# Kernel tuning notes

Measured on AMD Instinct MI355X. Metric: run time of the kernel, lower is better.

## Reference

```python
import jax, jax.numpy as jnp
import numpy as np

C = 1024
KSIZE = 7
PAD = 3
STRIDE = 1


def _dwconv(x, w):
    # x: [B, C, L], w: [C, 1, K] depthwise (feature_group_count=C)
    return jax.lax.conv_general_dilated(
        x, w,
        window_strides=(STRIDE,),
        padding=[(PAD, PAD)],
        feature_group_count=C,
        dimension_numbers=('NCH', 'OIH', 'NCH'),
    )


def setup_inputs() -> dict:
    key = jax.random.key(0)
    kx, kq, kk, kv = jax.random.split(key, 4)
    B, L = 8, 4096
    x = jax.random.normal(kx, (B, C, L), dtype=jnp.float32)
    # depthwise conv weights, fan_in = 1*K per group -> kaiming-ish scale
    scale = 1.0 / np.sqrt(KSIZE)
    q_w = jax.random.normal(kq, (C, 1, KSIZE), dtype=jnp.float32) * scale
    k_w = jax.random.normal(kk, (C, 1, KSIZE), dtype=jnp.float32) * scale
    v_w = jax.random.normal(kv, (C, 1, KSIZE), dtype=jnp.float32) * scale
    return {"x": x, "q_w": q_w, "k_w": k_w, "v_w": v_w}


def reference(x, q_w, k_w, v_w):
    sqrt_dk = np.sqrt(C).astype(np.float32)
    q = _dwconv(x, q_w)  # [B, C, L']
    k = _dwconv(x, k_w)
    v = _dwconv(x, v_w)
    score = jnp.einsum('bcl,bdl->bcd', q, k) / sqrt_dk  # [B, C, C]
    attn = jax.nn.softmax(score, axis=-1)
    out = jnp.einsum('bcd,bdl->bcl', attn, v)  # [B, C, L']
    return out
```

## Files before the change

### kernel.cpp

```cpp
#include <hip/hip_runtime.h>
#include <hip/hip_bf16.h>

typedef unsigned short u16;
typedef __attribute__((ext_vector_type(8))) __bf16 bf16x8;
typedef __attribute__((ext_vector_type(4))) float f32x4;

#define CC 1024
#define LL 4096
#define NB 8

#define VMCNT(n) asm volatile("s_waitcnt vmcnt(" #n ")" ::: "memory")
#define BAR()    asm volatile("s_barrier" ::: "memory")

__device__ __forceinline__ u16 f2bf(float f) {
  union { float f; unsigned u; } v; v.f = f;
  unsigned u = v.u;
  return (u16)((u + 0x7fffu + ((u >> 16) & 1u)) >> 16);
}

__device__ __forceinline__ void gload_lds16(const void* g, void* l) {
  __builtin_amdgcn_global_load_lds(
      (const __attribute__((address_space(1))) void*)g,
      (__attribute__((address_space(3))) void*)l, 16, 0, 0);
}

__global__ __launch_bounds__(256) void dwconv_qkv(
    const float* __restrict__ x, const float* __restrict__ qw,
    const float* __restrict__ kw, const float* __restrict__ vw,
    u16* __restrict__ qo, u16* __restrict__ ko, u16* __restrict__ vto)
{
  __shared__ u16 vs[64][66];
  const int t  = threadIdx.x;
  const int l0 = blockIdx.x << 6;
  const int c0 = blockIdx.y << 6;
  const int b  = blockIdx.z;
  const int cc  = t >> 2;
  const int li0 = (t & 3) << 4;
  const int c   = c0 + cc;
  const float* xr = x + ((size_t)(b * CC + c)) * LL;
  const int p0 = l0 + li0;

  float xv[24];
  if (l0 != 0 && l0 != LL - 64) {
    const float4* base = (const float4*)(xr + p0 - 4);
#pragma unroll
    for (int j = 0; j < 6; ++j) {
      float4 f = base[j];
      xv[4 * j + 0] = f.x; xv[4 * j + 1] = f.y;
      xv[4 * j + 2] = f.z; xv[4 * j + 3] = f.w;
    }
  } else {
#pragma unroll
    for (int i = 0; i < 24; ++i) {
      int gl = p0 - 4 + i;
      xv[i] = ((unsigned)gl < (unsigned)LL) ? xr[gl] : 0.f;
    }
  }

  float wq[7], wk[7], wv[7];
#pragma unroll
  for (int j = 0; j < 7; ++j) {
    wq[j] = qw[c * 7 + j]; wk[j] = kw[c * 7 + j]; wv[j] = vw[c * 7 + j];
  }

  alignas(16) u16 qv[16], kv[16];
#pragma unroll
  for (int li = 0; li < 16; ++li) {
    float aq = 0.f, ak = 0.f, av = 0.f;
#pragma unroll
    for (int j = 0; j < 7; ++j) {
      float xf = xv[li + 1 + j];
      aq = fmaf(xf, wq[j], aq);
      ak = fmaf(xf, wk[j], ak);
      av = fmaf(xf, wv[j], av);
    }
    qv[li] = f2bf(aq);
    kv[li] = f2bf(ak);
    vs[li0 + li][cc] = f2bf(av);
  }
  size_t qoff = ((size_t)(b * CC + c)) * LL + p0;
  *(uint4*)(qo + qoff)     = ((const uint4*)qv)[0];
  *(uint4*)(qo + qoff + 8) = ((const uint4*)qv)[1];
  *(uint4*)(ko + qoff)     = ((const uint4*)kv)[0];
  *(uint4*)(ko + qoff + 8) = ((const uint4*)kv)[1];

  __syncthreads();
  const int ll = t >> 2;
  const int cg = (t & 3) << 4;
  alignas(16) u16 vr[16];
#pragma unroll
  for (int j = 0; j < 16; ++j) vr[j] = vs[ll][cg + j];
  size_t voff = ((size_t)(b * LL + l0 + ll)) * CC + c0 + cg;
  *(uint4*)(vto + voff)     = ((const uint4*)vr)[0];
  *(uint4*)(vto + voff + 8) = ((const uint4*)vr)[1];
}

__global__ __launch_bounds__(512, 2) void gemm256p(
    const u16* __restrict__ A, int lda, size_t sA,
    const u16* __restrict__ B, int ldb, size_t sB,
    float* __restrict__ C0, float* __restrict__ C1, int ldc, size_t sC,
    int K, int ksplit, int mapmode)
{
  __shared__ alignas(16) u16 lds[65536];
  const int t    = threadIdx.x;
  const int lane = t & 63, wave = t >> 6;
  const int wrow = wave >> 2, wcol = wave & 3;
  int bx, by, z;
  if (mapmode == 0) {
    int wg = blockIdx.x; z = wg & 15; int r = wg >> 4; bx = r & 3; by = r >> 2;
  } else {
    int wg = blockIdx.x; z = wg & 7; by = (wg >> 3) & 3; bx = wg >> 5;
  }
  const int bm = by << 8, bn = bx << 8;
  const int batch = (ksplit == 2) ? (z >> 1) : z;
  const int split = (ksplit == 2) ? (z & 1) : 0;
  const int Ks    = (ksplit == 2) ? (K >> 1) : K;
  const u16* Ab = A + (size_t)batch * sA + (size_t)split * Ks;
  const u16* Bb = B + (size_t)batch * sB + (size_t)split * Ks;

  const int srow = lane >> 3;
  const int scol = ((lane & 7) ^ srow) << 3;
  const u16* pA[2][2]; const u16* pB[2][2];
  int dstOff[2];
#pragma unroll
  for (int i = 0; i < 2; ++i) {
    int c = wave * 2 + i;
    dstOff[i] = c * 1024 + lane * 16;
    pA[0][i] = Ab + (size_t)(bm + c * 8 + srow) * lda + scol;
    pA[1][i] = pA[0][i] + (size_t)128 * lda;
    pB[0][i] = Bb + (size_t)(bn + c * 8 + srow) * ldb + scol;
    pB[1][i] = pB[0][i] + (size_t)128 * ldb;
  }

#define STGH(P, h, base, koff)                                            \
  do {                                                                    \
    gload_lds16(P[h][0] + (koff), (char*)lds + (base) + dstOff[0]);       \
    gload_lds16(P[h][1] + (koff), (char*)lds + (base) + dstOff[1]);       \
  } while (0)

  const int r15 = lane & 15, kq = lane >> 4, swz = r15 & 7;
  int rowA[8], rowB[4], colK[2];
#pragma unroll
  for (int m = 0; m < 8; ++m) rowA[m] = (wrow * 128 + m * 16 + r15) * 128;
#pragma unroll
  for (int n = 0; n < 4; ++n) rowB[n] = 32768 + (wcol * 64 + n * 16 + r15) * 128;
#pragma unroll
  for (int s = 0; s < 2; ++s) colK[s] = (((s * 4 + kq) ^ swz)) << 4;

  f32x4 acc[8][4];
#pragma unroll
  for (int i = 0; i < 8; ++i)
#pragma unroll
    for (int j = 0; j < 4; ++j) acc[i][j] = f32x4{0.f, 0.f, 0.f, 0.f};

  const int NT = Ks >> 6;

  STGH(pA, 0, 0, 0);            STGH(pA, 1, 16384, 0);
  STGH(pB, 0, 32768, 0);        STGH(pB, 1, 49152, 0);
  STGH(pA, 0, 65536 + 0, 64);   STGH(pA, 1, 65536 + 16384, 64);
  STGH(pB, 0, 65536 + 32768, 64);
  VMCNT(6);
  BAR();

  const char* L = (const char*)lds;
  for (int tt = 0; tt < NT; ++tt) {
    const int d = tt & 1;
    const int dbase = d << 16, sbase = (d ^ 1) << 16;
    const int kN1 = (tt + 1) << 6, kN2 = (tt + 2) << 6;
    bf16x8 a0[4], aK1a[4], b0[4];
#pragma unroll
    for (int m = 0; m < 4; ++m) {
      a0[m]   = *(const bf16x8*)(L + dbase + rowA[m] + colK[0]);
      aK1a[m] = *(const bf16x8*)(L + dbase + rowA[m] + colK[1]);
    }
#pragma unroll
    for (int n = 0; n < 4; ++n) b0[n] = *(const bf16x8*)(L + dbase + rowB[n] + colK[0]);
    if (tt + 1 < NT) STGH(pB, 1, sbase + 49152, kN1);
    __builtin_amdgcn_s_setprio(1);
#pragma unroll
    for (int m = 0; m < 4; ++m)
#pragma unroll
      for (int n = 0; n < 4; ++n)
        acc[m][n] = __builtin_amdgcn_mfma_f32_16x16x32_bf16(a0[m], b0[n], acc[m][n], 0, 0, 0);
    __builtin_amdgcn_s_setprio(0);
    bf16x8 a4[4], aK1b[4];
#pragma unroll
    for (int m = 0; m < 4; ++m) {
      a4[m]   = *(const bf16x8*)(L + dbase + rowA[m + 4] + colK[0]);
      aK1b[m] = *(const bf16x8*)(L + dbase + rowA[m + 4] + colK[1]);
    }
    __builtin_amdgcn_s_setprio(1);
#pragma unroll
    for (int m = 0; m < 4; ++m)
#pragma unroll
      for (int n = 0; n < 4; ++n)
        acc[m + 4][n] = __builtin_amdgcn_mfma_f32_16x16x32_bf16(a4[m], b0[n], acc[m + 4][n], 0, 0, 0);
    __builtin_amdgcn_s_setprio(0);
    BAR();
    bf16x8 b1[4];
#pragma unroll
    for (int n = 0; n < 4; ++n) b1[n] = *(const bf16x8*)(L + dbase + rowB[n] + colK[1]);
    if (tt + 2 < NT) STGH(pA, 0, dbase + 0, kN2);
    __builtin_amdgcn_s_setprio(1);
#pragma unroll
    for (int m = 0; m < 4; ++m)
#pragma unroll
      for (int n = 0; n < 4; ++n)
        acc[m][n] = __builtin_amdgcn_mfma_f32_16x16x32_bf16(aK1a[m], b1[n], acc[m][n], 0, 0, 0);
    __builtin_amdgcn_s_setprio(0);
    BAR();
    if (tt + 2 < NT) { STGH(pA, 1, dbase + 16384, kN2); STGH(pB, 0, dbase + 32768, kN2); }
    __builtin_amdgcn_s_setprio(1);
#pragma unroll
    for (int m = 0; m < 4; ++m)
#pragma unroll
      for (int n = 0; n < 4; ++n)
        acc[m + 4][n] = __builtin_amdgcn_mfma_f32_16x16x32_bf16(aK1b[m], b1[n], acc[m + 4][n], 0, 0, 0);
    __builtin_amdgcn_s_setprio(0);
    if (tt < NT - 2) { VMCNT(6); } else { VMCNT(0); }
    BAR();
  }
#undef STGH

  float* Cb = (split ? C1 : C0) + (size_t)batch * sC;
  const int row0 = bm + wrow * 128 + kq * 4;
  const int col0 = bn + wcol * 64 + r15;
#pragma unroll
  for (int m = 0; m < 8; ++m)
#pragma unroll
    for (int n = 0; n < 4; ++n) {
      const int r   = row0 + m * 16;
      const int col = col0 + n * 16;
#pragma unroll
      for (int rr = 0; rr < 4; ++rr)
        Cb[(size_t)(r + rr) * ldc + col] = acc[m][n][rr];
    }
}

__global__ __launch_bounds__(256) void softmax_rows(
    float* __restrict__ score, const float* __restrict__ part)
{
  __shared__ float rmax[4], rsum[4];
  const int t = threadIdx.x;
  const int lane = t & 63, wv = t >> 6;
  float* sp = score + ((size_t)blockIdx.x << 10);
  const float* pp = part + ((size_t)blockIdx.x << 10);
  float4 v = ((const float4*)sp)[t];
  float4 w = ((const float4*)pp)[t];
  const float scale = 0.03125f;
  float a0 = (v.x + w.x) * scale, a1 = (v.y + w.y) * scale;
  float a2 = (v.z + w.z) * scale, a3 = (v.w + w.w) * scale;
  float m = fmaxf(fmaxf(a0, a1), fmaxf(a2, a3));
#pragma unroll
  for (int o = 1; o < 64; o <<= 1) m = fmaxf(m, __shfl_xor(m, o, 64));
  if (lane == 0) rmax[wv] = m;
  __syncthreads();
  m = fmaxf(fmaxf(rmax[0], rmax[1]), fmaxf(rmax[2], rmax[3]));
  float e0 = __expf(a0 - m), e1 = __expf(a1 - m);
  float e2 = __expf(a2 - m), e3 = __expf(a3 - m);
  float s = e0 + e1 + e2 + e3;
#pragma unroll
  for (int o = 1; o < 64; o <<= 1) s += __shfl_xor(s, o, 64);
  if (lane == 0) rsum[wv] = s;
  __syncthreads();
  s = rsum[0] + rsum[1] + rsum[2] + rsum[3];
  const float inv = 1.0f / s;
  union { u16 u[4]; uint2 p; } ob;
  ob.u[0] = f2bf(e0 * inv); ob.u[1] = f2bf(e1 * inv);
  ob.u[2] = f2bf(e2 * inv); ob.u[3] = f2bf(e3 * inv);
  *(uint2*)((u16*)sp + (t << 2)) = ob.p;
}

extern "C" void kernel_launch(void* const* d_in, const int* in_sizes, int n_in,
                              void* d_out, int out_size, void* d_ws, size_t ws_size,
                              hipStream_t stream) {
  const float* x  = (const float*)d_in[0];
  const float* qw = (const float*)d_in[1];
  const float* kw = (const float*)d_in[2];
  const float* vw = (const float*)d_in[3];
  float* out = (float*)d_out;
  char* ws = (char*)d_ws;

  u16*  q      = (u16*)ws;
  u16*  k      = (u16*)(ws + 67108864);
  u16*  vt     = (u16*)(ws + 134217728);
  float* score = (float*)(ws + 201326592);
  float* part  = out;

  dim3 cg(LL / 64, CC / 64, NB);
  dwconv_qkv<<<cg, 256, 0, stream>>>(x, qw, kw, vw, q, k, vt);

  gemm256p<<<dim3(256), 512, 0, stream>>>(q, LL, (size_t)CC * LL,
                                          k, LL, (size_t)CC * LL,
                                          score, part, CC, (size_t)CC * CC,
                                          LL, 2, 0);

  softmax_rows<<<NB * CC, 256, 0, stream>>>(score, part);

  gemm256p<<<dim3(512), 512, 0, stream>>>((const u16*)score, 2048, (size_t)CC * 2048,
                                          vt, CC, (size_t)LL * CC,
                                          out, nullptr, LL, (size_t)CC * LL,
                                          CC, 1, 1);
}
```

Measured before the change: 251.5 us.

## Widen dwconv tiles, swizzle V transpose, use hardware bf16 convert and nontemporal stores

The depthwise conv kernel now covers 128 sequence positions per block instead of 64, with 32 outputs per thread. This cuts halo reloads and the number of blocks. The shared-memory transpose for V uses an XOR swizzle on 16-column groups to reduce bank conflicts, and each thread writes 64-byte rows of V^T. The manual bf16 rounding is replaced with the compiler's native conversion. Q, K, V^T and the GEMM outputs are written with nontemporal stores to reduce cache pollution, at the cost of more registers per thread and possibly worse reuse when later kernels read the data.

Result: slower. 466.1 us (+85.4%).

```diff
diff --git a/kernel.cpp b/kernel.cpp
--- a/kernel.cpp
+++ b/kernel.cpp
@@ -4,6 +4,7 @@
 typedef unsigned short u16;
 typedef __attribute__((ext_vector_type(8))) __bf16 bf16x8;
 typedef __attribute__((ext_vector_type(4))) float f32x4;
+typedef __attribute__((ext_vector_type(4))) unsigned int u32x4;
 
 #define CC 1024
 #define LL 4096
@@ -16,6 +17,11 @@
   union { float f; unsigned u; } v; v.f = f;
   unsigned u = v.u;
   return (u16)((u + 0x7fffu + ((u >> 16) & 1u)) >> 16);
+}
+
+__device__ __forceinline__ u16 bfc(float f) {
+  __bf16 h = (__bf16)f;
+  return __builtin_bit_cast(u16, h);
 }
 
 __device__ __forceinline__ void gload_lds16(const void* g, void* l) {
@@ -29,29 +35,29 @@
     const float* __restrict__ kw, const float* __restrict__ vw,
     u16* __restrict__ qo, u16* __restrict__ ko, u16* __restrict__ vto)
 {
-  __shared__ u16 vs[64][66];
+  __shared__ u16 vs[128][68];
   const int t  = threadIdx.x;
-  const int l0 = blockIdx.x << 6;
+  const int l0 = blockIdx.x << 7;
   const int c0 = blockIdx.y << 6;
   const int b  = blockIdx.z;
-  const int cc  = t >> 2;
-  const int li0 = (t & 3) << 4;
-  const int c   = c0 + cc;
+  const int cc = t >> 2;
+  const int g  = t & 3;
+  const int c  = c0 + cc;
   const float* xr = x + ((size_t)(b * CC + c)) * LL;
-  const int p0 = l0 + li0;
-
-  float xv[24];
-  if (l0 != 0 && l0 != LL - 64) {
+  const int p0 = l0 + (g << 5);
+
+  float xv[40];
+  if (l0 != 0 && l0 != LL - 128) {
     const float4* base = (const float4*)(xr + p0 - 4);
 #pragma unroll
-    for (int j = 0; j < 6; ++j) {
+    for (int j = 0; j < 10; ++j) {
       float4 f = base[j];
       xv[4 * j + 0] = f.x; xv[4 * j + 1] = f.y;
       xv[4 * j + 2] = f.z; xv[4 * j + 3] = f.w;
     }
   } else {
 #pragma unroll
-    for (int i = 0; i < 24; ++i) {
+    for (int i = 0; i < 40; ++i) {
       int gl = p0 - 4 + i;
       xv[i] = ((unsigned)gl < (unsigned)LL) ? xr[gl] : 0.f;
     }
@@ -63,9 +69,10 @@
     wq[j] = qw[c * 7 + j]; wk[j] = kw[c * 7 + j]; wv[j] = vw[c * 7 + j];
   }
 
-  alignas(16) u16 qv[16], kv[16];
-#pragma unroll
-  for (int li = 0; li < 16; ++li) {
+  const int wgrp = cc >> 4;
+  alignas(16) u16 qv[32], kv[32];
+#pragma unroll
+  for (int li = 0; li < 32; ++li) {
     float aq = 0.f, ak = 0.f, av = 0.f;
 #pragma unroll
     for (int j = 0; j < 7; ++j) {
@@ -74,25 +81,33 @@
       ak = fmaf(xf, wk[j], ak);
       av = fmaf(xf, wv[j], av);
     }
-    qv[li] = f2bf(aq);
-    kv[li] = f2bf(ak);
-    vs[li0 + li][cc] = f2bf(av);
+    qv[li] = bfc(aq);
+    kv[li] = bfc(ak);
+    vs[(g << 5) + li][(cc & 15) + ((wgrp ^ g) << 4)] = bfc(av);
   }
   size_t qoff = ((size_t)(b * CC + c)) * LL + p0;
-  *(uint4*)(qo + qoff)     = ((const uint4*)qv)[0];
-  *(uint4*)(qo + qoff + 8) = ((const uint4*)qv)[1];
-  *(uint4*)(ko + qoff)     = ((const uint4*)kv)[0];
-  *(uint4*)(ko + qoff + 8) = ((const uint4*)kv)[1];
+#pragma unroll
+  for (int h = 0; h < 4; ++h) {
+    __builtin_nontemporal_store(((const u32x4*)qv)[h], (u32x4*)(qo + qoff) + h);
+    __builtin_nontemporal_store(((const u32x4*)kv)[h], (u32x4*)(ko + qoff) + h);
+  }
 
   __syncthreads();
-  const int ll = t >> 2;
-  const int cg = (t & 3) << 4;
-  alignas(16) u16 vr[16];
-#pragma unroll
-  for (int j = 0; j < 16; ++j) vr[j] = vs[ll][cg + j];
-  size_t voff = ((size_t)(b * LL + l0 + ll)) * CC + c0 + cg;
-  *(uint4*)(vto + voff)     = ((const uint4*)vr)[0];
-  *(uint4*)(vto + voff + 8) = ((const uint4*)vr)[1];
+  const int ll   = t >> 1;
+  const int half = t & 1;
+  const int gll  = ll >> 5;
+  alignas(16) u16 vr[32];
+#pragma unroll
+  for (int bb = 0; bb < 2; ++bb) {
+    const int sb = ((half << 1) | bb) ^ gll;
+#pragma unroll
+    for (int j = 0; j < 16; ++j)
+      vr[bb * 16 + j] = vs[ll][(sb << 4) + j];
+  }
+  size_t voff = ((size_t)(b * LL) + l0 + ll) * CC + c0 + (half << 5);
+#pragma unroll
+  for (int h = 0; h < 4; ++h)
+    __builtin_nontemporal_store(((const u32x4*)vr)[h], (u32x4*)(vto + voff) + h);
 }
 
 __global__ __launch_bounds__(512, 2) void gemm256p(
@@ -124,11 +139,11 @@
   int dstOff[2];
 #pragma unroll
   for (int i = 0; i < 2; ++i) {
-    int c = wave * 2 + i;
-    dstOff[i] = c * 1024 + lane * 16;
-    pA[0][i] = Ab + (size_t)(bm + c * 8 + srow) * lda + scol;
+    int cch = wave * 2 + i;
+    dstOff[i] = cch * 1024 + lane * 16;
+    pA[0][i] = Ab + (size_t)(bm + cch * 8 + srow) * lda + scol;
     pA[1][i] = pA[0][i] + (size_t)128 * lda;
-    pB[0][i] = Bb + (size_t)(bn + c * 8 + srow) * ldb + scol;
+    pB[0][i] = Bb + (size_t)(bn + cch * 8 + srow) * ldb + scol;
     pB[1][i] = pB[0][i] + (size_t)128 * ldb;
   }
 
@@ -233,7 +248,7 @@
       const int col = col0 + n * 16;
 #pragma unroll
       for (int rr = 0; rr < 4; ++rr)
-        Cb[(size_t)(r + rr) * ldc + col] = acc[m][n][rr];
+        __builtin_nontemporal_store(acc[m][n][rr], &Cb[(size_t)(r + rr) * ldc + col]);
     }
 }
 
@@ -287,7 +302,7 @@
   float* score = (float*)(ws + 201326592);
   float* part  = out;
 
-  dim3 cg(LL / 64, CC / 64, NB);
+  dim3 cg(LL / 128, CC / 64, NB);
   dwconv_qkv<<<cg, 256, 0, stream>>>(x, qw, kw, vw, q, k, vt);
 
   gemm256p<<<dim3(256), 512, 0, stream>>>(q, LL, (size_t)CC * LL,
```
